# Kernel optimization log

Hardware: AMD Instinct MI355X
Metric: run time of the kernel (lower is better)

Reference implementation:

```python
import jax, jax.numpy as jnp
import numpy as np

# Per-type input feature dims (NODE_DIM values); max dim = 128 = padded width of x.
NODE_DIMS = np.array([16, 32, 64, 128, 64, 32, 16, 128], dtype=np.int32)
N_TYPES = 8
MAX_DIM = 128
FEAT = 256          # node_feature_dim
N_GRAPHS = 100000   # batch_size; one node of each type per graph


def setup_inputs() -> dict:
    key = jax.random.key(0)
    k1, k2, k3 = jax.random.split(key, 3)
    num_nodes = N_GRAPHS * N_TYPES
    x = jax.random.normal(k1, (num_nodes, MAX_DIM), dtype=jnp.float32)
    # Per-type Linear weights, padded to MAX_DIM on the input axis.
    W = jax.random.normal(k2, (N_TYPES, FEAT, MAX_DIM), dtype=jnp.float32) * 0.05
    b = jax.random.normal(k3, (N_TYPES, FEAT), dtype=jnp.float32) * 0.05
    return {"x": x, "W": W, "b": b}


def reference(x, W, b):
    # Node n = g*N_TYPES + k is the type-k node of graph g (the gather index
    # ptr[b] + node_name.index(k) in the original). Dropout is eval-mode (identity).
    # Mask weight columns beyond each type's true input dim: equivalent to
    # slicing x[:, :NODE_DIM[k]] before the per-type Linear.
    mask = (jnp.arange(MAX_DIM)[None, None, :] < jnp.asarray(NODE_DIMS)[:, None, None]).astype(x.dtype)  # [T,1,D]
    W_eff = W * mask  # [T,F,D]
    xg = x.reshape(N_GRAPHS, N_TYPES, MAX_DIM)  # [G,T,D]
    y = jnp.einsum("gtd,tfd->gtf", xg, W_eff) + b[None, :, :]  # [G,T,F]
    return y.reshape(N_GRAPHS * N_TYPES, FEAT)
```

## Files before the change

### kernel.cpp

```cpp
#include <hip/hip_runtime.h>

#define N_GRAPHS 100000
#define NTYPES 8
#define MAXD 128
#define FEAT 256
#define NB 2
#define GPW (16 * NB)
#define LDR 68

typedef __attribute__((ext_vector_type(8))) short short8;
typedef __attribute__((ext_vector_type(4))) float f32x4;
typedef __attribute__((ext_vector_type(4))) unsigned uint4v;

constexpr int KSN[NTYPES]  = {1, 1, 2, 4, 2, 1, 1, 4};
constexpr int DIMS[NTYPES] = {16, 32, 64, 128, 64, 32, 16, 128};

__device__ __forceinline__ unsigned f2bf_u(float f) {
    unsigned u = __builtin_bit_cast(unsigned, f);
    return (u + 0x7fffu + ((u >> 16) & 1u)) >> 16;
}
__device__ __forceinline__ unsigned cvt2(float lo, float hi) {
    return f2bf_u(lo) | (f2bf_u(hi) << 16);
}
__device__ __forceinline__ f32x4 cvt8f(f32x4 a, f32x4 b) {
    uint4v u;
    u.x = cvt2(a.x, a.y); u.y = cvt2(a.z, a.w);
    u.z = cvt2(b.x, b.y); u.w = cvt2(b.z, b.w);
    return __builtin_bit_cast(f32x4, u);
}

__global__ __launch_bounds__(256)
void prepack_w(const float* __restrict__ W, short8* __restrict__ wp)
{
    const int idx  = blockIdx.x * 256 + threadIdx.x;
    const int c16  = idx & 15;
    const int cgrp = (idx >> 4) & 3;
    const int ks   = (idx >> 6) & 3;
    const int ct   = (idx >> 8) & 15;
    const int t    = (idx >> 12) & 7;
    const int col  = ct * 16 + c16;
    const int k    = ks * 32 + cgrp * 8;
    const int dim  = 16 << ((0x30123210u >> (4 * t)) & 0xf);
    const float* src = W + ((size_t)t * FEAT + col) * MAXD + k;
    f32x4 a = *(const f32x4*)src;
    f32x4 b = *(const f32x4*)(src + 4);
    #pragma unroll
    for (int j = 0; j < 4; ++j) {
        if (k + j     >= dim) a[j] = 0.f;
        if (k + 4 + j >= dim) b[j] = 0.f;
    }
    f32x4 r = cvt8f(a, b);
    *(f32x4*)&wp[idx] = r;
}

template<int T, bool PRE>
__device__ __forceinline__ void do_type(const float* __restrict__ x,
                                        const short8* __restrict__ wp,
                                        const float* __restrict__ W,
                                        const float* __restrict__ bias_g,
                                        float* __restrict__ out,
                                        float* __restrict__ buf,
                                        int g0, int lane, int cgrp, int c16)
{
    constexpr int KS = KSN[T];

    short8 a[NB][KS];
    #pragma unroll
    for (int b = 0; b < NB; ++b)
        #pragma unroll
        for (int ks = 0; ks < KS; ++ks) {
            f32x4 tmp = *(const f32x4*)&buf[(b * 16 + c16) * LDR + ks * 16 + cgrp * 4];
            a[b][ks] = __builtin_bit_cast(short8, tmp);
        }

    #pragma unroll
    for (int ct4 = 0; ct4 < 4; ++ct4) {
        #pragma unroll
        for (int c = 0; c < 4; ++c) {
            const int ct = ct4 * 4 + c;
            short8 wf[KS];
            if constexpr (PRE) {
                #pragma unroll
                for (int ks = 0; ks < KS; ++ks)
                    wf[ks] = wp[(((T * 16 + ct) * 4 + ks) * 4 + cgrp) * 16 + c16];
            } else {
                constexpr int DIM = DIMS[T];
                #pragma unroll
                for (int ks = 0; ks < KS; ++ks) {
                    const int k = ks * 32 + cgrp * 8;
                    const float* wfp = W + ((size_t)T * FEAT + ct * 16 + c16) * MAXD + k;
                    f32x4 wa = *(const f32x4*)wfp;
                    f32x4 wb = *(const f32x4*)(wfp + 4);
                    #pragma unroll
                    for (int j = 0; j < 4; ++j) {
                        if (k + j     >= DIM) wa[j] = 0.f;
                        if (k + 4 + j >= DIM) wb[j] = 0.f;
                    }
                    wf[ks] = __builtin_bit_cast(short8, cvt8f(wa, wb));
                }
            }
            #pragma unroll
            for (int b = 0; b < NB; ++b) {
                f32x4 acc = {0.f, 0.f, 0.f, 0.f};
                #pragma unroll
                for (int ks = 0; ks < KS; ++ks)
                    acc = __builtin_amdgcn_mfma_f32_16x16x32_bf16(a[b][ks], wf[ks], acc, 0, 0, 0);
                #pragma unroll
                for (int r = 0; r < 4; ++r)
                    buf[(b * 16 + cgrp * 4 + r) * LDR + c * 16 + c16] = acc[r];
            }
        }
        #pragma unroll
        for (int i = 0; i < 8; ++i) {
            const int row   = i * 4 + (lane >> 4);
            const int coldw = (lane & 15) * 4;
            f32x4 v  = *(const f32x4*)&buf[row * LDR + coldw];
            f32x4 b4 = *(const f32x4*)&bias_g[T * FEAT + ct4 * 64 + coldw];
            f32x4 res;
            #pragma unroll
            for (int r = 0; r < 4; ++r) res[r] = v[r] + b4[r];
            __builtin_nontemporal_store(res,
                (f32x4*)&out[(((size_t)(g0 + row)) * NTYPES + T) * FEAT + ct4 * 64 + coldw]);
        }
    }

    if constexpr (T + 1 < NTYPES) {
        constexpr int KSn  = KSN[T + 1];
        constexpr int SPRn = KSn * 4;
        #pragma unroll
        for (int p = 0; p < 2 * KSn; ++p) {
            const int idx = p * 64 + lane;
            const int row = idx / SPRn, s8 = idx % SPRn;
            const float* rp = x + (((size_t)(g0 + row)) * NTYPES + (T + 1)) * MAXD + s8 * 8;
            f32x4 v0 = __builtin_nontemporal_load((const f32x4*)rp);
            f32x4 v1 = __builtin_nontemporal_load((const f32x4*)rp + 1);
            *(f32x4*)&buf[row * LDR + s8 * 4] = cvt8f(v0, v1);
        }
        do_type<T + 1, PRE>(x, wp, W, bias_g, out, buf, g0, lane, cgrp, c16);
    }
}

template<bool PRE>
__global__ __launch_bounds__(256, 4)
void node_enc(const float* __restrict__ x, const short8* __restrict__ wp,
              const float* __restrict__ W, const float* __restrict__ bias_g,
              float* __restrict__ out)
{
    __shared__ __align__(16) float Buf[4][GPW * LDR];
    const int tid  = threadIdx.x;
    const int lane = tid & 63;
    const int wave = tid >> 6;
    const int cgrp = lane >> 4;
    const int c16  = lane & 15;
    const int w    = blockIdx.x * 4 + wave;
    if (w >= N_GRAPHS / GPW) return;
    const int g0   = w * GPW;

    float* buf = Buf[wave];
    #pragma unroll
    for (int p = 0; p < 2; ++p) {
        const int idx = p * 64 + lane;
        const int row = idx >> 2, s8 = idx & 3;
        const float* rp = x + (((size_t)(g0 + row)) * NTYPES + 0) * MAXD + s8 * 8;
        f32x4 v0 = __builtin_nontemporal_load((const f32x4*)rp);
        f32x4 v1 = __builtin_nontemporal_load((const f32x4*)rp + 1);
        *(f32x4*)&buf[row * LDR + s8 * 4] = cvt8f(v0, v1);
    }

    do_type<0, PRE>(x, wp, W, bias_g, out, buf, g0, lane, cgrp, c16);
}

extern "C" void kernel_launch(void* const* d_in, const int* in_sizes, int n_in,
                              void* d_out, int out_size, void* d_ws, size_t ws_size,
                              hipStream_t stream)
{
    const float* x = (const float*)d_in[0];
    const float* W = (const float*)d_in[1];
    const float* b = (const float*)d_in[2];
    float* out = (float*)d_out;

    const int grid = (N_GRAPHS / GPW + 3) / 4;
    const size_t wp_bytes = (size_t)32768 * sizeof(short8);

    if (ws_size >= wp_bytes) {
        short8* wp = (short8*)d_ws;
        prepack_w<<<128, 256, 0, stream>>>(W, wp);
        node_enc<true><<<grid, 256, 0, stream>>>(x, wp, W, b, out);
    } else {
        node_enc<false><<<grid, 256, 0, stream>>>(x, nullptr, W, b, out);
    }
}
```

Measured before the change: 325.6 us.

## Split LDS into separate bf16 A-tile and fp32 epilogue buffers, batch weight loads

Replaces the shared fp32 staging buffer that held both the bf16 A operands and the MFMA outputs with a dedicated bf16 A-tile buffer and a smaller per-16-row epilogue buffer. The A tile no longer has to be fully consumed into registers before outputs overwrite it. Weight fragments for four column tiles are loaded up front before the MFMAs, and the epilogue is emitted per 16-row batch. Minimum occupancy in launch bounds drops from 4 to 3 to leave room for the extra registers, which may reduce latency hiding.

```diff
diff --git a/kernel.cpp b/kernel.cpp
--- a/kernel.cpp
+++ b/kernel.cpp
@@ -6,7 +6,8 @@
 #define FEAT 256
 #define NB 2
 #define GPW (16 * NB)
-#define LDR 68
+#define ALDA 136
+#define ELDA 68
 
 typedef __attribute__((ext_vector_type(8))) short short8;
 typedef __attribute__((ext_vector_type(4))) float f32x4;
@@ -22,11 +23,11 @@
 __device__ __forceinline__ unsigned cvt2(float lo, float hi) {
     return f2bf_u(lo) | (f2bf_u(hi) << 16);
 }
-__device__ __forceinline__ f32x4 cvt8f(f32x4 a, f32x4 b) {
+__device__ __forceinline__ short8 cvt8(f32x4 a, f32x4 b) {
     uint4v u;
     u.x = cvt2(a.x, a.y); u.y = cvt2(a.z, a.w);
     u.z = cvt2(b.x, b.y); u.w = cvt2(b.z, b.w);
-    return __builtin_bit_cast(f32x4, u);
+    return __builtin_bit_cast(short8, u);
 }
 
 __global__ __launch_bounds__(256)
@@ -49,8 +50,7 @@
         if (k + j     >= dim) a[j] = 0.f;
         if (k + 4 + j >= dim) b[j] = 0.f;
     }
-    f32x4 r = cvt8f(a, b);
-    *(f32x4*)&wp[idx] = r;
+    wp[idx] = cvt8(a, b);
 }
 
 template<int T, bool PRE>
@@ -59,7 +59,8 @@
                                         const float* __restrict__ W,
                                         const float* __restrict__ bias_g,
                                         float* __restrict__ out,
-                                        float* __restrict__ buf,
+                                        unsigned short* __restrict__ as_,
+                                        float* __restrict__ ep,
                                         int g0, int lane, int cgrp, int c16)
 {
     constexpr int KS = KSN[T];
@@ -68,21 +69,19 @@
     #pragma unroll
     for (int b = 0; b < NB; ++b)
         #pragma unroll
-        for (int ks = 0; ks < KS; ++ks) {
-            f32x4 tmp = *(const f32x4*)&buf[(b * 16 + c16) * LDR + ks * 16 + cgrp * 4];
-            a[b][ks] = __builtin_bit_cast(short8, tmp);
-        }
+        for (int ks = 0; ks < KS; ++ks)
+            a[b][ks] = *(const short8*)&as_[(b * 16 + c16) * ALDA + ks * 32 + cgrp * 8];
 
     #pragma unroll
     for (int ct4 = 0; ct4 < 4; ++ct4) {
+        short8 wf4[4][KS];
         #pragma unroll
         for (int c = 0; c < 4; ++c) {
             const int ct = ct4 * 4 + c;
-            short8 wf[KS];
             if constexpr (PRE) {
                 #pragma unroll
                 for (int ks = 0; ks < KS; ++ks)
-                    wf[ks] = wp[(((T * 16 + ct) * 4 + ks) * 4 + cgrp) * 16 + c16];
+                    wf4[c][ks] = wp[(((T * 16 + ct) * 4 + ks) * 4 + cgrp) * 16 + c16];
             } else {
                 constexpr int DIM = DIMS[T];
                 #pragma unroll
@@ -96,31 +95,34 @@
                         if (k + j     >= DIM) wa[j] = 0.f;
                         if (k + 4 + j >= DIM) wb[j] = 0.f;
                     }
-                    wf[ks] = __builtin_bit_cast(short8, cvt8f(wa, wb));
+                    wf4[c][ks] = cvt8(wa, wb);
                 }
             }
+        }
+        #pragma unroll
+        for (int b = 0; b < NB; ++b) {
             #pragma unroll
-            for (int b = 0; b < NB; ++b) {
+            for (int c = 0; c < 4; ++c) {
                 f32x4 acc = {0.f, 0.f, 0.f, 0.f};
                 #pragma unroll
                 for (int ks = 0; ks < KS; ++ks)
-                    acc = __builtin_amdgcn_mfma_f32_16x16x32_bf16(a[b][ks], wf[ks], acc, 0, 0, 0);
+                    acc = __builtin_amdgcn_mfma_f32_16x16x32_bf16(a[b][ks], wf4[c][ks], acc, 0, 0, 0);
                 #pragma unroll
                 for (int r = 0; r < 4; ++r)
-                    buf[(b * 16 + cgrp * 4 + r) * LDR + c * 16 + c16] = acc[r];
+                    ep[(cgrp * 4 + r) * ELDA + c * 16 + c16] = acc[r];
             }
-        }
-        #pragma unroll
-        for (int i = 0; i < 8; ++i) {
-            const int row   = i * 4 + (lane >> 4);
-            const int coldw = (lane & 15) * 4;
-            f32x4 v  = *(const f32x4*)&buf[row * LDR + coldw];
-            f32x4 b4 = *(const f32x4*)&bias_g[T * FEAT + ct4 * 64 + coldw];
-            f32x4 res;
             #pragma unroll
-            for (int r = 0; r < 4; ++r) res[r] = v[r] + b4[r];
-            __builtin_nontemporal_store(res,
-                (f32x4*)&out[(((size_t)(g0 + row)) * NTYPES + T) * FEAT + ct4 * 64 + coldw]);
+            for (int i = 0; i < 4; ++i) {
+                const int row   = i * 4 + (lane >> 4);
+                const int coldw = (lane & 15) * 4;
+                f32x4 v  = *(const f32x4*)&ep[row * ELDA + coldw];
+                f32x4 b4 = *(const f32x4*)&bias_g[T * FEAT + ct4 * 64 + coldw];
+                f32x4 res;
+                #pragma unroll
+                for (int r = 0; r < 4; ++r) res[r] = v[r] + b4[r];
+                __builtin_nontemporal_store(res,
+                    (f32x4*)&out[(((size_t)(g0 + b * 16 + row)) * NTYPES + T) * FEAT + ct4 * 64 + coldw]);
+            }
         }
     }
 
@@ -134,19 +136,20 @@
             const float* rp = x + (((size_t)(g0 + row)) * NTYPES + (T + 1)) * MAXD + s8 * 8;
             f32x4 v0 = __builtin_nontemporal_load((const f32x4*)rp);
             f32x4 v1 = __builtin_nontemporal_load((const f32x4*)rp + 1);
-            *(f32x4*)&buf[row * LDR + s8 * 4] = cvt8f(v0, v1);
+            *(short8*)&as_[row * ALDA + s8 * 8] = cvt8(v0, v1);
         }
-        do_type<T + 1, PRE>(x, wp, W, bias_g, out, buf, g0, lane, cgrp, c16);
+        do_type<T + 1, PRE>(x, wp, W, bias_g, out, as_, ep, g0, lane, cgrp, c16);
     }
 }
 
 template<bool PRE>
-__global__ __launch_bounds__(256, 4)
+__global__ __launch_bounds__(256, 3)
 void node_enc(const float* __restrict__ x, const short8* __restrict__ wp,
               const float* __restrict__ W, const float* __restrict__ bias_g,
               float* __restrict__ out)
 {
-    __shared__ __align__(16) float Buf[4][GPW * LDR];
+    __shared__ __align__(16) unsigned short As[4][GPW * ALDA];
+    __shared__ __align__(16) float          Ep[4][16 * ELDA];
     const int tid  = threadIdx.x;
     const int lane = tid & 63;
     const int wave = tid >> 6;
@@ -156,7 +159,7 @@
     if (w >= N_GRAPHS / GPW) return;
     const int g0   = w * GPW;
 
-    float* buf = Buf[wave];
+    unsigned short* as_ = As[wave];
     #pragma unroll
     for (int p = 0; p < 2; ++p) {
         const int idx = p * 64 + lane;
@@ -164,10 +167,10 @@
         const float* rp = x + (((size_t)(g0 + row)) * NTYPES + 0) * MAXD + s8 * 8;
         f32x4 v0 = __builtin_nontemporal_load((const f32x4*)rp);
         f32x4 v1 = __builtin_nontemporal_load((const f32x4*)rp + 1);
-        *(f32x4*)&buf[row * LDR + s8 * 4] = cvt8f(v0, v1);
+        *(short8*)&as_[row * ALDA + s8 * 8] = cvt8(v0, v1);
     }
 
-    do_type<0, PRE>(x, wp, W, bias_g, out, buf, g0, lane, cgrp, c16);
+    do_type<0, PRE>(x, wp, W, bias_g, out, as_, Ep[wave], g0, lane, cgrp, c16);
 }
 
 extern "C" void kernel_launch(void* const* d_in, const int* in_sizes, int n_in,
```

Result: faster. 309.8 us (-4.9%).
